# Kernel tuning notes

Measured on AMD Instinct MI355X. Metric: run time of the kernel, lower is better.

Reference implementation:

```python
import jax, jax.numpy as jnp
import numpy as np

B, P, HID = 2, 4096, 1152
N_HEADS, HEAD_DIM = 16, 72
EPS = 1e-6


def _rms_norm(x, w=None):
    # x fp32; normalize over last dim
    ms = jnp.mean(x * x, axis=-1, keepdims=True) + EPS
    y = x * jax.lax.rsqrt(ms)
    if w is not None:
        y = y * w
    return y


def _rotate_half(x):
    d = x.shape[-1] // 2
    return jnp.concatenate([-x[..., d:], x[..., :d]], axis=-1)


def _apply_rotary(x, c, s):
    # x: [B,P,N,d], c/s: [B,P,d] -> broadcast over heads
    c = c[:, :, None, :]
    s = s[:, :, None, :]
    return x * c + _rotate_half(x) * s


def _multidim_rope(x, cos, sin, ndim=2):
    per = x.shape[-1] // ndim
    parts = []
    for k in range(ndim):
        sl = slice(k * per, (k + 1) * per)
        parts.append(_apply_rotary(x[..., sl], cos[..., sl], sin[..., sl]))
    return jnp.concatenate(parts, axis=-1)


def setup_inputs() -> dict:
    key = jax.random.key(0)
    ks = jax.random.split(key, 8)
    return {
        "hidden_states": jax.random.normal(ks[0], (B, P, HID), jnp.float32),
        "cos": jax.random.normal(ks[1], (B, P, HEAD_DIM), jnp.float32),
        "sin": jax.random.normal(ks[2], (B, P, HEAD_DIM), jnp.float32),
        "Wq": jax.random.normal(ks[3], (HID, N_HEADS * HEAD_DIM), jnp.float32) * 0.02,
        "Wk": jax.random.normal(ks[4], (HID, N_HEADS * HEAD_DIM), jnp.float32) * 0.02,
        "Wv": jax.random.normal(ks[5], (HID, N_HEADS * HEAD_DIM), jnp.float32) * 0.02,
        "Wo": jax.random.normal(ks[6], (N_HEADS * HEAD_DIM, HID), jnp.float32) * 0.02,
        "q_norm_w": jnp.ones((HEAD_DIM,), jnp.float32),
        "k_norm_w": jnp.ones((HEAD_DIM,), jnp.float32),
    }


def reference(hidden_states, cos, sin, Wq, Wk, Wv, Wo, q_norm_w, k_norm_w):
    b, p, _ = hidden_states.shape
    q = (hidden_states @ Wq).reshape(b, p, N_HEADS, HEAD_DIM)
    k = (hidden_states @ Wk).reshape(b, p, N_HEADS, HEAD_DIM)
    v = (hidden_states @ Wv).reshape(b, p, N_HEADS, HEAD_DIM)
    # per-head RMSNorm (q/k with learned scale, v without)
    q = _rms_norm(q, q_norm_w)
    k = _rms_norm(k, k_norm_w)
    v = _rms_norm(v)
    # multi-dim RoPE (ndim=2)
    q = _multidim_rope(q, cos, sin)
    k = _multidim_rope(k, cos, sin)
    # attention, scaling = 1.0, no mask (non-causal vision)
    scores = jnp.einsum('bqnd,bknd->bnqk', q, k)  # [B,N,P,P]
    attn = jax.nn.softmax(scores.astype(jnp.float32), axis=-1).astype(q.dtype)
    out = jnp.einsum('bnqk,bknd->bqnd', attn, v).reshape(b, p, N_HEADS * HEAD_DIM)
    return out @ Wo
```

## Files before the change

kernel.cpp:

```cpp
#include <hip/hip_runtime.h>
#include <stdint.h>

typedef __attribute__((ext_vector_type(8))) _Float16 half8;
typedef __attribute__((ext_vector_type(4))) _Float16 half4;
typedef __attribute__((ext_vector_type(4))) float floatx4;

#define NHEADS 16
#define HDIM   72
#define DPAD   80
#define DPADV  80
#define HID    1152
#define NQKV   3456
#define PP     4096
#define MR     8192

__device__ __forceinline__ float bf2f(unsigned short u) {
  union { unsigned int i; float f; } c; c.i = ((unsigned int)u) << 16; return c.f;
}
__device__ __forceinline__ unsigned short f2bf(float f) {
  union { float f; unsigned int i; } c; c.f = f;
  unsigned int x = c.i;
  x += ((x >> 16) & 1u) + 0x7fffu;
  return (unsigned short)(x >> 16);
}
__device__ __forceinline__ float load_in(const void* p, long long i, int bf) {
  return bf ? bf2f(((const unsigned short*)p)[i]) : ((const float*)p)[i];
}

__global__ __launch_bounds__(64) void k_detect(const void* hs, int* flag) {
  int lane = threadIdx.x;
  const unsigned short* u = (const unsigned short*)hs;
  int wild = 0;
  for (int t = 0; t < 8; ++t) {
    unsigned short v = u[lane * 8 + t];
    int e = (v >> 7) & 0xFF;
    if (e >= 134) wild++;
  }
  for (int off = 1; off < 64; off <<= 1) wild += __shfl_xor(wild, off);
  if (lane == 0) flag[0] = (wild > 32) ? 0 : 1;
}

__global__ __launch_bounds__(256) void k_prep(
    const void* hs, const void* cosp, const void* sinp,
    const void* wq, const void* wk, const void* wv, const void* wo,
    const void* qnw, const void* knw, const int* flag,
    _Float16* Xh, _Float16* Wqkv, _Float16* Wot,
    float* cosf, float* sinf, float* qw, float* kw) {
  int bf = flag[0];
  long long i = (long long)blockIdx.x * blockDim.x + threadIdx.x;
  const long long n0 = (long long)MR * HID;
  const long long n1 = (long long)NQKV * HID;
  const long long n2 = (long long)HID * HID;
  const long long n3 = (long long)2 * PP * HDIM;
  if (i < n0) { Xh[i] = (_Float16)load_in(hs, i, bf); return; }
  i -= n0;
  if (i < n1) {
    long long n = i / HID, kk = i - n * HID;
    int sel = (int)(n / HID);
    long long nl = n - (long long)sel * HID;
    const void* W = (sel == 0) ? wq : ((sel == 1) ? wk : wv);
    Wqkv[i] = (_Float16)load_in(W, kk * HID + nl, bf);
    return;
  }
  i -= n1;
  if (i < n2) {
    long long n = i / HID, kk = i - n * HID;
    Wot[i] = (_Float16)load_in(wo, kk * HID + n, bf);
    return;
  }
  i -= n2;
  if (i < n3) { cosf[i] = load_in(cosp, i, bf); return; }
  i -= n3;
  if (i < n3) { sinf[i] = load_in(sinp, i, bf); return; }
  i -= n3;
  if (i < HDIM) { qw[i] = load_in(qnw, i, bf); return; }
  i -= HDIM;
  if (i < HDIM) { kw[i] = load_in(knw, i, bf); return; }
}

#define LDA 40
__global__ __launch_bounds__(256) void k_gemm(
    const _Float16* __restrict__ A, const _Float16* __restrict__ Bt,
    int N, int K, int mode, const int* __restrict__ flag,
    void* __restrict__ outp) {
  __shared__ _Float16 As[128 * LDA];
  __shared__ _Float16 Bs[128 * LDA];
  int tid = threadIdx.x;
  int wave = tid >> 6, lane = tid & 63;
  int quad = lane >> 4, l16 = lane & 15;
  int bM = blockIdx.y * 128, bN = blockIdx.x * 128;
  int wm = (wave & 1) * 64, wn = (wave >> 1) * 64;
  int qk = quad * 8;
  int sr = tid >> 1, sc = (tid & 1) * 16;

  floatx4 acc[4][4];
  floatx4 z4 = {0.f, 0.f, 0.f, 0.f};
#pragma unroll
  for (int i = 0; i < 4; ++i)
#pragma unroll
    for (int j = 0; j < 4; ++j) acc[i][j] = z4;

  const _Float16* gA = A + (size_t)(bM + sr) * K + sc;
  const _Float16* gB = Bt + (size_t)(bN + sr) * K + sc;

  for (int k0 = 0; k0 < K; k0 += 32) {
    half8 a0 = *(const half8*)(gA);
    half8 a1 = *(const half8*)(gA + 8);
    half8 b0 = *(const half8*)(gB);
    half8 b1 = *(const half8*)(gB + 8);
    gA += 32; gB += 32;
    __syncthreads();
    *(half8*)(As + sr * LDA + sc)     = a0;
    *(half8*)(As + sr * LDA + sc + 8) = a1;
    *(half8*)(Bs + sr * LDA + sc)     = b0;
    *(half8*)(Bs + sr * LDA + sc + 8) = b1;
    __syncthreads();
    half8 af[4], bfv[4];
#pragma unroll
    for (int i = 0; i < 4; ++i)
      af[i] = *(const half8*)(As + (wm + i * 16 + l16) * LDA + qk);
#pragma unroll
    for (int j = 0; j < 4; ++j)
      bfv[j] = *(const half8*)(Bs + (wn + j * 16 + l16) * LDA + qk);
#pragma unroll
    for (int i = 0; i < 4; ++i)
#pragma unroll
      for (int j = 0; j < 4; ++j)
        acc[i][j] = __builtin_amdgcn_mfma_f32_16x16x32_f16(af[i], bfv[j], acc[i][j], 0, 0, 0);
  }

  if (mode == 0) {
#pragma unroll
    for (int i = 0; i < 4; ++i)
#pragma unroll
      for (int j = 0; j < 4; ++j)
#pragma unroll
        for (int r = 0; r < 4; ++r) {
          size_t row = (size_t)(bM + wm + i * 16 + quad * 4 + r);
          size_t col = (size_t)(bN + wn + j * 16 + l16);
          ((_Float16*)outp)[row * N + col] = (_Float16)acc[i][j][r];
        }
  } else {
    int obf = flag[0];
#pragma unroll
    for (int i = 0; i < 4; ++i)
#pragma unroll
      for (int j = 0; j < 4; ++j)
#pragma unroll
        for (int r = 0; r < 4; ++r) {
          size_t row = (size_t)(bM + wm + i * 16 + quad * 4 + r);
          size_t col = (size_t)(bN + wn + j * 16 + l16);
          float v = acc[i][j][r];
          if (obf) ((unsigned short*)outp)[row * N + col] = f2bf(v);
          else     ((float*)outp)[row * N + col] = v;
        }
  }
}

__global__ __launch_bounds__(256) void k_norm_rope(
    const _Float16* __restrict__ QKV, const float* __restrict__ cosf,
    const float* __restrict__ sinf, const float* __restrict__ qw,
    const float* __restrict__ kw,
    _Float16* __restrict__ Qp, _Float16* __restrict__ Kp,
    _Float16* __restrict__ Vp) {
  int wave = threadIdx.x >> 6, lane = threadIdx.x & 63;
  int bid = blockIdx.x * 4 + wave;
  int m = bid >> 4, h = bid & 15;
  int b = m >> 12, p = m & 4095;
  __shared__ float sq[4][HDIM], sk[4][HDIM];

  const _Float16* rowp = QKV + (long long)m * NQKV + h * HDIM;
  int i0 = lane, i1 = lane + 64;
  bool has1 = (i1 < HDIM);
  float q0 = (float)rowp[i0];
  float k0 = (float)rowp[1152 + i0];
  float v0 = (float)rowp[2304 + i0];
  float q1 = 0.f, k1 = 0.f, v1 = 0.f;
  if (has1) { q1 = (float)rowp[i1]; k1 = (float)rowp[1152 + i1]; v1 = (float)rowp[2304 + i1]; }

  float sq_s = q0 * q0 + q1 * q1;
  float sk_s = k0 * k0 + k1 * k1;
  float sv_s = v0 * v0 + v1 * v1;
  for (int off = 1; off < 64; off <<= 1) {
    sq_s += __shfl_xor(sq_s, off);
    sk_s += __shfl_xor(sk_s, off);
    sv_s += __shfl_xor(sv_s, off);
  }
  float rq = rsqrtf(sq_s / 72.f + 1e-6f);
  float rk = rsqrtf(sk_s / 72.f + 1e-6f);
  float rv = rsqrtf(sv_s / 72.f + 1e-6f);

  sq[wave][i0] = q0 * rq * qw[i0];
  sk[wave][i0] = k0 * rk * kw[i0];
  if (has1) { sq[wave][i1] = q1 * rq * qw[i1]; sk[wave][i1] = k1 * rk * kw[i1]; }
  __syncthreads();

  const float* crow = cosf + (long long)m * HDIM;
  const float* srow = sinf + (long long)m * HDIM;
  long long obase = ((long long)(b * NHEADS + h) * PP + p) * DPAD;
  long long obV   = ((long long)(b * NHEADS + h) * PP + p) * DPADV;
#pragma unroll
  for (int t = 0; t < 2; ++t) {
    int i = lane + t * 64;
    if (i < DPAD) {
      _Float16 qv = (_Float16)0.f, kv = (_Float16)0.f;
      if (i < HDIM) {
        int j = (i >= 36) ? (i - 36) : i;
        float c = crow[i], s = srow[i];
        float qo, ko;
        if (j < 18) { qo = sq[wave][i] * c - sq[wave][i + 18] * s; ko = sk[wave][i] * c - sk[wave][i + 18] * s; }
        else        { qo = sq[wave][i] * c + sq[wave][i - 18] * s; ko = sk[wave][i] * c + sk[wave][i - 18] * s; }
        qv = (_Float16)qo; kv = (_Float16)ko;
      }
      Qp[obase + i] = qv; Kp[obase + i] = kv;
    }
    if (i < DPADV) {
      _Float16 vv = (_Float16)0.f;
      if (i < HDIM) vv = (_Float16)(((t == 0) ? v0 : v1) * rv);
      Vp[obV + i] = vv;
    }
  }
}

__global__ __launch_bounds__(256) void k_vtrans(
    const _Float16* __restrict__ Vp, _Float16* __restrict__ VtG) {
  __shared__ _Float16 T[DPADV * 72];
  int tid = threadIdx.x;
  int pt = blockIdx.x, bh = blockIdx.y;
  long long src = (long long)bh * PP * DPADV + (long long)pt * 64 * DPADV;
#pragma unroll
  for (int pp = 0; pp < 3; ++pp) {
    int c = tid + pp * 256;
    if (c < 640) {
      int r = c / 10, ds = c % 10;
      half8 v = *(const half8*)(Vp + src + r * DPADV + ds * 8);
#pragma unroll
      for (int j = 0; j < 8; ++j) T[(ds * 8 + j) * 72 + r] = v[j];
    }
  }
  __syncthreads();
  long long dst = (long long)bh * DPADV * PP + (long long)pt * 64;
#pragma unroll
  for (int pp = 0; pp < 3; ++pp) {
    int c = tid + pp * 256;
    if (c < 640) {
      int d = c >> 3, ps = (c & 7) * 8;
      half8 v = *(const half8*)(T + d * 72 + ps);
      if (d == 72) {
#pragma unroll
        for (int j = 0; j < 8; ++j) v[j] = (_Float16)1.f;
      }
      *(half8*)(VtG + dst + (long long)d * PP + ps) = v;
    }
  }
}

#define TK 64
#define NT (PP / TK)
#define LDK 80
#define LDV 72
__global__ __launch_bounds__(256) void k_flash(
    const _Float16* __restrict__ Qp, const _Float16* __restrict__ Kp,
    const _Float16* __restrict__ VtG, _Float16* __restrict__ Oat) {
  __shared__ _Float16 Kl[TK * LDK];
  __shared__ _Float16 Vt[DPADV * LDV];
  __shared__ _Float16 Pl[128 * LDV];
  int tid = threadIdx.x, wave = tid >> 6, lane = tid & 63;
  int quad = lane >> 4, l16 = lane & 15;
  int bh = blockIdx.x, qt = blockIdx.y;
  const long long headoff = (long long)bh * PP * DPAD;
  const long long vhead   = (long long)bh * DPADV * PP;

  half8 zh8;
#pragma unroll
  for (int j = 0; j < 8; ++j) zh8[j] = (_Float16)0.f;

  half8 qf[2][3];
#pragma unroll
  for (int mb = 0; mb < 2; ++mb) {
    int qrow = qt * 128 + wave * 32 + mb * 16 + l16;
    const _Float16* qp = Qp + headoff + (long long)qrow * DPAD;
#pragma unroll
    for (int ck = 0; ck < 2; ++ck)
      qf[mb][ck] = *(const half8*)(qp + ck * 32 + quad * 8);
    qf[mb][2] = zh8;
    if (quad < 2) qf[mb][2] = *(const half8*)(qp + 64 + quad * 8);
  }

  floatx4 O[2][5];
  floatx4 z4 = {0.f, 0.f, 0.f, 0.f};
#pragma unroll
  for (int mb = 0; mb < 2; ++mb)
#pragma unroll
    for (int d = 0; d < 5; ++d) O[mb][d] = z4;
  float m_i[2];
  m_i[0] = -1e30f; m_i[1] = -1e30f;
  _Float16* Pw = Pl + wave * 32 * LDV;

  half8 kreg[3], vreg[3];
  {
    const _Float16* Ksrc = Kp + headoff;
    const _Float16* Vsrc = VtG + vhead;
#pragma unroll
    for (int pp = 0; pp < 3; ++pp) {
      int c = tid + pp * 256;
      if (c < 640)
        kreg[pp] = *(const half8*)(Ksrc + c * 8);
    }
#pragma unroll
    for (int pp = 0; pp < 3; ++pp) {
      int c = tid + pp * 256;
      if (c < 640)
        vreg[pp] = *(const half8*)(Vsrc + (long long)(c >> 3) * PP + (c & 7) * 8);
    }
  }

  for (int kt = 0; kt < NT; ++kt) {
    __syncthreads();
#pragma unroll
    for (int pp = 0; pp < 3; ++pp) {
      int c = tid + pp * 256;
      if (c < 640)
        *(half8*)(Kl + (c / 10) * LDK + (c % 10) * 8) = kreg[pp];
    }
#pragma unroll
    for (int pp = 0; pp < 3; ++pp) {
      int c = tid + pp * 256;
      if (c < 640)
        *(half8*)(Vt + (c >> 3) * LDV + (c & 7) * 8) = vreg[pp];
    }
    __syncthreads();

    {
      int ktn = (kt + 1 < NT) ? kt + 1 : kt;
      const _Float16* Ksrc = Kp + headoff + (long long)ktn * TK * DPAD;
      const _Float16* Vsrc = VtG + vhead + ktn * TK;
#pragma unroll
      for (int pp = 0; pp < 3; ++pp) {
        int c = tid + pp * 256;
        if (c < 640)
          kreg[pp] = *(const half8*)(Ksrc + c * 8);
      }
#pragma unroll
      for (int pp = 0; pp < 3; ++pp) {
        int c = tid + pp * 256;
        if (c < 640)
          vreg[pp] = *(const half8*)(Vsrc + (long long)(c >> 3) * PP + (c & 7) * 8);
      }
    }

    floatx4 sb[2][4];
    __builtin_amdgcn_s_setprio(1);
#pragma unroll
    for (int nb = 0; nb < 4; ++nb) {
      const _Float16* kp = Kl + (nb * 16 + l16) * LDK;
      half8 kf0 = *(const half8*)(kp + quad * 8);
      half8 kf1 = *(const half8*)(kp + 32 + quad * 8);
      half8 kf2 = zh8;
      if (quad < 2) kf2 = *(const half8*)(kp + 64 + quad * 8);
#pragma unroll
      for (int mb = 0; mb < 2; ++mb) {
        floatx4 a = __builtin_amdgcn_mfma_f32_16x16x32_f16(kf0, qf[mb][0], z4, 0, 0, 0);
        a = __builtin_amdgcn_mfma_f32_16x16x32_f16(kf1, qf[mb][1], a, 0, 0, 0);
        a = __builtin_amdgcn_mfma_f32_16x16x32_f16(kf2, qf[mb][2], a, 0, 0, 0);
        sb[mb][nb] = a;
      }
    }
    __builtin_amdgcn_s_setprio(0);

#pragma unroll
    for (int mb = 0; mb < 2; ++mb) {
      float t = fmaxf(fmaxf(sb[mb][0][0], sb[mb][0][1]),
                      fmaxf(sb[mb][0][2], sb[mb][0][3]));
#pragma unroll
      for (int nb = 1; nb < 4; ++nb)
        t = fmaxf(t, fmaxf(fmaxf(sb[mb][nb][0], sb[mb][nb][1]),
                           fmaxf(sb[mb][nb][2], sb[mb][nb][3])));
      t = fmaxf(t, __shfl_xor(t, 16));
      t = fmaxf(t, __shfl_xor(t, 32));
      if (!__all(t <= m_i[mb] + 8.f)) {
        float mnew = fmaxf(m_i[mb], t);
        float al = __expf(m_i[mb] - mnew);
        m_i[mb] = mnew;
        float alT[4];
#pragma unroll
        for (int r = 0; r < 4; ++r)
          alT[r] = __shfl(al, (lane & 48) + quad * 4 + r);
#pragma unroll
        for (int d = 0; d < 5; ++d)
#pragma unroll
          for (int r = 0; r < 4; ++r) O[mb][d][r] *= alT[r];
      }
      float mi = m_i[mb];
#pragma unroll
      for (int nb = 0; nb < 4; ++nb) {
        half4 w;
#pragma unroll
        for (int r = 0; r < 4; ++r)
          w[r] = (_Float16)__expf(sb[mb][nb][r] - mi);
        *(half4*)(Pw + (mb * 16 + l16) * LDV + nb * 16 + quad * 4) = w;
      }
    }

    __builtin_amdgcn_s_setprio(1);
#pragma unroll
    for (int ck2 = 0; ck2 < 2; ++ck2) {
      half8 pf0 = *(const half8*)(Pw + l16 * LDV + ck2 * 32 + quad * 8);
      half8 pf1 = *(const half8*)(Pw + (16 + l16) * LDV + ck2 * 32 + quad * 8);
#pragma unroll
      for (int d = 0; d < 5; ++d) {
        half8 vf = *(const half8*)(Vt + (d * 16 + l16) * LDV + ck2 * 32 + quad * 8);
        O[0][d] = __builtin_amdgcn_mfma_f32_16x16x32_f16(pf0, vf, O[0][d], 0, 0, 0);
        O[1][d] = __builtin_amdgcn_mfma_f32_16x16x32_f16(pf1, vf, O[1][d], 0, 0, 0);
      }
    }
    __builtin_amdgcn_s_setprio(0);
  }

  int b = bh >> 4, h = bh & 15;
  int src = (lane & 48) + 8;
#pragma unroll
  for (int mb = 0; mb < 2; ++mb) {
    float linv[4];
#pragma unroll
    for (int r = 0; r < 4; ++r)
      linv[r] = 1.f / __shfl(O[mb][4][r], src);
    long long orow = (long long)b * PP + qt * 128 + wave * 32 + mb * 16 + quad * 4;
#pragma unroll
    for (int d = 0; d < 5; ++d) {
      int dd = d * 16 + l16;
      if (dd < HDIM) {
#pragma unroll
        for (int r = 0; r < 4; ++r)
          Oat[(orow + r) * HID + h * HDIM + dd] = (_Float16)(O[mb][d][r] * linv[r]);
      }
    }
  }
}

extern "C" void kernel_launch(void* const* d_in, const int* in_sizes, int n_in,
                              void* d_out, int out_size, void* d_ws, size_t ws_size,
                              hipStream_t stream) {
  (void)in_sizes; (void)n_in; (void)out_size; (void)ws_size;
  const void* hs   = d_in[0];
  const void* cosp = d_in[1];
  const void* sinp = d_in[2];
  const void* wq   = d_in[3];
  const void* wk   = d_in[4];
  const void* wv   = d_in[5];
  const void* wo   = d_in[6];
  const void* qnw  = d_in[7];
  const void* knw  = d_in[8];

  char* ws = (char*)d_ws;
  size_t off = 0;
  auto take = [&](size_t bytes) -> char* {
    off = (off + 255) & ~(size_t)255;
    char* p = ws + off; off += bytes; return p;
  };
  int* flag        = (int*)take(4);
  _Float16* Xh     = (_Float16*)take((size_t)MR * HID * 2);
  _Float16* Wqkvh  = (_Float16*)take((size_t)NQKV * HID * 2);
  _Float16* Woth   = (_Float16*)take((size_t)HID * HID * 2);
  float* cosf_     = (float*)take((size_t)2 * PP * HDIM * 4);
  float* sinf_     = (float*)take((size_t)2 * PP * HDIM * 4);
  float* qwf       = (float*)take(HDIM * 4);
  float* kwf       = (float*)take(HDIM * 4);
  _Float16* QKVh   = (_Float16*)take((size_t)MR * NQKV * 2);
  _Float16* Kp     = (_Float16*)take((size_t)2 * NHEADS * PP * DPAD * 2);
  _Float16* Vp     = (_Float16*)take((size_t)2 * NHEADS * PP * DPADV * 2);
  _Float16* Qp  = Xh;
  _Float16* Oat = QKVh;
  _Float16* VtG = (_Float16*)((char*)QKVh + (size_t)20 * 1024 * 1024);

  k_detect<<<dim3(1), dim3(64), 0, stream>>>(hs, flag);

  long long totalPrep = (long long)MR * HID + (long long)NQKV * HID +
                        (long long)HID * HID + 2LL * 2 * PP * HDIM + 2 * HDIM;
  int prepBlocks = (int)((totalPrep + 255) / 256);
  k_prep<<<dim3(prepBlocks), dim3(256), 0, stream>>>(
      hs, cosp, sinp, wq, wk, wv, wo, qnw, knw, flag,
      Xh, Wqkvh, Woth, cosf_, sinf_, qwf, kwf);

  k_gemm<<<dim3(NQKV / 128, MR / 128), dim3(256), 0, stream>>>(
      Xh, Wqkvh, NQKV, HID, 0, flag, QKVh);

  k_norm_rope<<<dim3(MR * NHEADS / 4), dim3(256), 0, stream>>>(
      QKVh, cosf_, sinf_, qwf, kwf, Qp, Kp, Vp);

  k_vtrans<<<dim3(PP / 64, 2 * NHEADS), dim3(256), 0, stream>>>(Vp, VtG);

  k_flash<<<dim3(2 * NHEADS, PP / 128), dim3(256), 0, stream>>>(Qp, Kp, VtG, Oat);

  k_gemm<<<dim3(HID / 128, MR / 128), dim3(256), 0, stream>>>(
      Oat, Woth, HID, HID, 1, flag, d_out);
}
```

Baseline: 685.1 us.

## Use exp2 softmax with prescaled Q, XCD-aware GEMM swizzle, register prefetch

Q is prescaled by log2(e) in the norm/rope kernel so the attention softmax can use exp2f, which drops a multiply from every exponential, and the lazy-rescale threshold is widened to match the base-2 scale. The GEMM now remaps block indices so that each XCD works on a contiguous band of rows, which should improve L2 reuse. It also prefetches the next K tile's global loads into registers before the MFMA work so load latency overlaps with compute. The softmax threshold change alters when rescaling happens, and fp16 P values can reach larger magnitudes before a rescale.

```diff
diff --git a/kernel.cpp b/kernel.cpp
--- a/kernel.cpp
+++ b/kernel.cpp
@@ -13,6 +13,7 @@
 #define NQKV   3456
 #define PP     4096
 #define MR     8192
+#define LOG2E  1.44269504f
 
 __device__ __forceinline__ float bf2f(unsigned short u) {
   union { unsigned int i; float f; } c; c.i = ((unsigned int)u) << 16; return c.f;
@@ -88,7 +89,16 @@
   int tid = threadIdx.x;
   int wave = tid >> 6, lane = tid & 63;
   int quad = lane >> 4, l16 = lane & 15;
-  int bM = blockIdx.y * 128, bN = blockIdx.x * 128;
+
+  int lin = blockIdx.y * gridDim.x + blockIdx.x;
+  int xcd = lin & 7;
+  int j = lin >> 3;
+  int nbx = gridDim.x;
+  int rows_per = gridDim.y >> 3;
+  int by = xcd * rows_per + j / nbx;
+  int bx = j - (j / nbx) * nbx;
+  int bM = by * 128, bN = bx * 128;
+
   int wm = (wave & 1) * 64, wn = (wave >> 1) * 64;
   int qk = quad * 8;
   int sr = tid >> 1, sc = (tid & 1) * 16;
@@ -98,59 +108,67 @@
 #pragma unroll
   for (int i = 0; i < 4; ++i)
 #pragma unroll
-    for (int j = 0; j < 4; ++j) acc[i][j] = z4;
+    for (int jj = 0; jj < 4; ++jj) acc[i][jj] = z4;
 
   const _Float16* gA = A + (size_t)(bM + sr) * K + sc;
   const _Float16* gB = Bt + (size_t)(bN + sr) * K + sc;
 
+  half8 a0 = *(const half8*)(gA);
+  half8 a1 = *(const half8*)(gA + 8);
+  half8 b0 = *(const half8*)(gB);
+  half8 b1 = *(const half8*)(gB + 8);
+  gA += 32; gB += 32;
+
   for (int k0 = 0; k0 < K; k0 += 32) {
-    half8 a0 = *(const half8*)(gA);
-    half8 a1 = *(const half8*)(gA + 8);
-    half8 b0 = *(const half8*)(gB);
-    half8 b1 = *(const half8*)(gB + 8);
-    gA += 32; gB += 32;
     __syncthreads();
     *(half8*)(As + sr * LDA + sc)     = a0;
     *(half8*)(As + sr * LDA + sc + 8) = a1;
     *(half8*)(Bs + sr * LDA + sc)     = b0;
     *(half8*)(Bs + sr * LDA + sc + 8) = b1;
     __syncthreads();
+    if (k0 + 32 < K) {
+      a0 = *(const half8*)(gA);
+      a1 = *(const half8*)(gA + 8);
+      b0 = *(const half8*)(gB);
+      b1 = *(const half8*)(gB + 8);
+      gA += 32; gB += 32;
+    }
     half8 af[4], bfv[4];
 #pragma unroll
     for (int i = 0; i < 4; ++i)
       af[i] = *(const half8*)(As + (wm + i * 16 + l16) * LDA + qk);
 #pragma unroll
-    for (int j = 0; j < 4; ++j)
-      bfv[j] = *(const half8*)(Bs + (wn + j * 16 + l16) * LDA + qk);
+    for (int jj = 0; jj < 4; ++jj)
+      bfv[jj] = *(const half8*)(Bs + (wn + jj * 16 + l16) * LDA + qk);
 #pragma unroll
     for (int i = 0; i < 4; ++i)
 #pragma unroll
-      for (int j = 0; j < 4; ++j)
-        acc[i][j] = __builtin_amdgcn_mfma_f32_16x16x32_f16(af[i], bfv[j], acc[i][j], 0, 0, 0);
+      for (int jj = 0; jj < 4; ++jj)
+        acc[i][jj] = __builtin_amdgcn_mfma_f32_16x16x32_f16(af[i], bfv[jj], acc[i][jj], 0, 0, 0);
   }
 
   if (mode == 0) {
 #pragma unroll
     for (int i = 0; i < 4; ++i)
 #pragma unroll
-      for (int j = 0; j < 4; ++j)
+      for (int jj = 0; jj < 4; ++jj)
 #pragma unroll
         for (int r = 0; r < 4; ++r) {
           size_t row = (size_t)(bM + wm + i * 16 + quad * 4 + r);
-          size_t col = (size_t)(bN + wn + j * 16 + l16);
-          ((_Float16*)outp)[row * N + col] = (_Float16)acc[i][j][r];
+          size_t col = (size_t)(bN + wn + jj * 16 + l16);
+          ((_Float16*)outp)[row * N + col] = (_Float16)acc[i][jj][r];
         }
   } else {
     int obf = flag[0];
 #pragma unroll
     for (int i = 0; i < 4; ++i)
 #pragma unroll
-      for (int j = 0; j < 4; ++j)
+      for (int jj = 0; jj < 4; ++jj)
 #pragma unroll
         for (int r = 0; r < 4; ++r) {
           size_t row = (size_t)(bM + wm + i * 16 + quad * 4 + r);
-          size_t col = (size_t)(bN + wn + j * 16 + l16);
-          float v = acc[i][j][r];
+          size_t col = (size_t)(bN + wn + jj * 16 + l16);
+          float v = acc[i][jj][r];
           if (obf) ((unsigned short*)outp)[row * N + col] = f2bf(v);
           else     ((float*)outp)[row * N + col] = v;
         }
@@ -210,7 +228,7 @@
         float qo, ko;
         if (j < 18) { qo = sq[wave][i] * c - sq[wave][i + 18] * s; ko = sk[wave][i] * c - sk[wave][i + 18] * s; }
         else        { qo = sq[wave][i] * c + sq[wave][i - 18] * s; ko = sk[wave][i] * c + sk[wave][i - 18] * s; }
-        qv = (_Float16)qo; kv = (_Float16)ko;
+        qv = (_Float16)(qo * LOG2E); kv = (_Float16)ko;
       }
       Qp[obase + i] = qv; Kp[obase + i] = kv;
     }
@@ -378,9 +396,9 @@
                            fmaxf(sb[mb][nb][2], sb[mb][nb][3])));
       t = fmaxf(t, __shfl_xor(t, 16));
       t = fmaxf(t, __shfl_xor(t, 32));
-      if (!__all(t <= m_i[mb] + 8.f)) {
+      if (!__all(t <= m_i[mb] + 11.5f)) {
         float mnew = fmaxf(m_i[mb], t);
-        float al = __expf(m_i[mb] - mnew);
+        float al = exp2f(m_i[mb] - mnew);
         m_i[mb] = mnew;
         float alT[4];
 #pragma unroll
@@ -397,7 +415,7 @@
         half4 w;
 #pragma unroll
         for (int r = 0; r < 4; ++r)
-          w[r] = (_Float16)__expf(sb[mb][nb][r] - mi);
+          w[r] = (_Float16)exp2f(sb[mb][nb][r] - mi);
         *(half4*)(Pw + (mb * 16 + l16) * LDV + nb * 16 + quad * 4) = w;
       }
     }
```

Result: faster. 658.2 us (-3.9%).
